# Kernel tuning notes

Measured on AMD Instinct MI355X. Metric: run time of the kernel, lower is better.

## Reference

```python
import jax, jax.numpy as jnp
import numpy as np

B, S, D, H = 4, 2048, 1024, 16
HD = D // H
SCALE = HD ** -0.5

def setup_inputs() -> dict:
    key = jax.random.key(0)
    k1, k2, k3 = jax.random.split(key, 3)
    x = jax.random.normal(k1, (B, S, D), dtype=jnp.float32)
    W_qkv = jax.random.normal(k2, (D, 3 * D), dtype=jnp.float32) * (D ** -0.5)
    b_qkv = jnp.zeros((3 * D,), dtype=jnp.float32)
    W_proj = jax.random.normal(k3, (D, D), dtype=jnp.float32) * (D ** -0.5)
    b_proj = jnp.zeros((D,), dtype=jnp.float32)
    return {"x": x, "W_qkv": W_qkv, "b_qkv": b_qkv, "W_proj": W_proj, "b_proj": b_proj}

def reference(x, W_qkv, b_qkv, W_proj, b_proj):
    # x: [B,S,D] -> qkv: [B,S,3D] -> [3,B,H,S,hd]
    qkv = x @ W_qkv + b_qkv
    qkv = qkv.reshape(B, S, 3, H, HD).transpose(2, 0, 3, 1, 4)
    q, k, v = qkv[0], qkv[1], qkv[2]
    # naive full attention: [B,H,S,S]
    attn = jnp.einsum('bhqd,bhkd->bhqk', q, k) * SCALE
    attn = jax.nn.softmax(attn, axis=-1)
    out = jnp.einsum('bhqk,bhkd->bhqd', attn, v)
    out = out.transpose(0, 2, 1, 3).reshape(B, S, D)
    return out @ W_proj + b_proj
```

## Files before the change

kernel.cpp:

```cpp
#include <hip/hip_runtime.h>

typedef __bf16 bf16x8 __attribute__((ext_vector_type(8)));
typedef unsigned short ushort8 __attribute__((ext_vector_type(8)));
typedef float floatx4 __attribute__((ext_vector_type(4)));
typedef unsigned int uintx4 __attribute__((ext_vector_type(4)));

__device__ __forceinline__ unsigned short f2bf(float f) {
  unsigned int u = __builtin_bit_cast(unsigned int, f);
  u += 0x7fffu + ((u >> 16) & 1u);
  return (unsigned short)(u >> 16);
}
__device__ __forceinline__ unsigned int pkbf(float a, float b) {
  unsigned int r;
  asm("v_cvt_pk_bf16_f32 %0, %1, %2" : "=v"(r) : "v"(a), "v"(b));
  return r;
}
__device__ __forceinline__ floatx4 MFMA16(bf16x8 a, bf16x8 b, floatx4 c) {
  return __builtin_amdgcn_mfma_f32_16x16x32_bf16(a, b, c, 0, 0, 0);
}

#define GLOAD16(gsrc, ldst)                                                  \
  __builtin_amdgcn_global_load_lds(                                          \
      (const __attribute__((address_space(1))) void*)(gsrc),                 \
      (__attribute__((address_space(3))) void*)(ldst), 16, 0, 0)

__global__ __launch_bounds__(256) void fill_f32(
    float* __restrict__ out, float val, size_t n) {
  const size_t t = (size_t)blockIdx.x * 256 + threadIdx.x;
  for (size_t i = t; i < n; i += (size_t)gridDim.x * 256) out[i] = val;
}

__global__ __launch_bounds__(256) void cvt_f32_bf16(
    const float* __restrict__ in, unsigned short* __restrict__ out) {
  const size_t t = (size_t)blockIdx.x * 256 + threadIdx.x;
  const float4 a = ((const float4*)in)[2 * t];
  const float4 b = ((const float4*)in)[2 * t + 1];
  uintx4 u;
  u[0] = pkbf(a.x, a.y); u[1] = pkbf(a.z, a.w);
  u[2] = pkbf(b.x, b.y); u[3] = pkbf(b.z, b.w);
  *(uintx4*)&out[t * 8] = u;
}

__global__ __launch_bounds__(256) void transpose_w(
    const float* __restrict__ in, unsigned short* __restrict__ out, int C) {
  __shared__ float T[64][65];
  const int tid = threadIdx.x;
  const int r0 = blockIdx.y * 64, c0 = blockIdx.x * 64;
#pragma unroll
  for (int e = 0; e < 4; ++e) {
    const int idx = e * 256 + tid;
    const int row = idx >> 4, cg = idx & 15;
    const float4 f = *(const float4*)&in[(size_t)(r0 + row) * C + c0 + cg * 4];
    T[row][cg * 4] = f.x; T[row][cg * 4 + 1] = f.y;
    T[row][cg * 4 + 2] = f.z; T[row][cg * 4 + 3] = f.w;
  }
  __syncthreads();
#pragma unroll
  for (int e = 0; e < 2; ++e) {
    const int idx = e * 256 + tid;
    const int cc = idx >> 3, rg = idx & 7;
    uintx4 u;
#pragma unroll
    for (int k = 0; k < 4; ++k)
      u[k] = pkbf(T[rg * 8 + 2 * k][cc], T[rg * 8 + 2 * k + 1][cc]);
    *(uintx4*)&out[(size_t)(c0 + cc) * 1024 + r0 + rg * 8] = u;
  }
}

template <int NBX, int EPI>
__global__ __launch_bounds__(512) void gemm8p(
    const unsigned short* __restrict__ A, const unsigned short* __restrict__ Bt,
    const float* __restrict__ bias, unsigned short* __restrict__ o0,
    unsigned short* __restrict__ o1, unsigned short* __restrict__ o2,
    float* __restrict__ of) {
  __shared__ __align__(16) unsigned short As[3][256 * 64];
  __shared__ __align__(16) unsigned short Bs[3][128 * 64];
  const int tid = threadIdx.x;
  const int lane = tid & 63;
  const int w = tid >> 6;
  const int g = lane >> 4, l15 = lane & 15;
  const int wr = w >> 1, wc = w & 1;
  constexpr int QX = 4 * NBX;
  const int orig = blockIdx.x;
  const int wgid = (orig & 7) * QX + (orig >> 3);
  const int m0 = (wgid / NBX) * 256, n0 = (wgid % NBX) * 128;

  floatx4 acc[4][4];
#pragma unroll
  for (int i = 0; i < 4; ++i)
#pragma unroll
    for (int j = 0; j < 4; ++j) acc[i][j] = {0.f, 0.f, 0.f, 0.f};

  const unsigned short* asrc[4];
  const unsigned short* bsrc[2];
  int adst[4], bdst[2];
#pragma unroll
  for (int p = 0; p < 4; ++p) {
    const int j = p * 512 + tid;
    const int row = j >> 3, G = j & 7;
    asrc[p] = A + (size_t)(m0 + row) * 1024 + (size_t)(G ^ (row & 7)) * 8;
    adst[p] = (j & ~63) * 8;
  }
#pragma unroll
  for (int p = 0; p < 2; ++p) {
    const int q = p * 512 + tid;
    const int row = q >> 3, G = q & 7;
    bsrc[p] = Bt + (size_t)(n0 + row) * 1024 + (size_t)(G ^ (row & 7)) * 8;
    bdst[p] = (q & ~63) * 8;
  }

  unsigned aoff[4][2], boff[4][2];
#pragma unroll
  for (int i = 0; i < 4; ++i) {
    const int ra = wr * 64 + i * 16 + l15;
    const int rb = wc * 64 + i * 16 + l15;
#pragma unroll
    for (int kh = 0; kh < 2; ++kh) {
      aoff[i][kh] = ra * 128 + (((kh * 4 + g) ^ (ra & 7)) * 16);
      boff[i][kh] = rb * 128 + (((kh * 4 + g) ^ (rb & 7)) * 16);
    }
  }

  auto STAGE = [&](int buf, int k0) {
#pragma unroll
    for (int p = 0; p < 4; ++p) GLOAD16(asrc[p] + k0, &As[buf][adst[p]]);
#pragma unroll
    for (int p = 0; p < 2; ++p) GLOAD16(bsrc[p] + k0, &Bs[buf][bdst[p]]);
  };
  auto COMPUTE = [&](int buf) {
    const char* ab = (const char*)As + buf * 32768;
    const char* bb = (const char*)Bs + buf * 16384;
#pragma unroll
    for (int kh = 0; kh < 2; ++kh) {
      bf16x8 af[4], bfr[4];
#pragma unroll
      for (int i = 0; i < 4; ++i) af[i] = *(const bf16x8*)(ab + aoff[i][kh]);
#pragma unroll
      for (int j = 0; j < 4; ++j) bfr[j] = *(const bf16x8*)(bb + boff[j][kh]);
      __builtin_amdgcn_s_setprio(1);
#pragma unroll
      for (int i = 0; i < 4; ++i)
#pragma unroll
        for (int j = 0; j < 4; ++j) acc[i][j] = MFMA16(af[i], bfr[j], acc[i][j]);
      __builtin_amdgcn_s_setprio(0);
    }
  };

  STAGE(0, 0);
  STAGE(1, 64);
#pragma unroll 1
  for (int t = 0; t < 16; ++t) {
    if (t < 14)
      asm volatile("s_waitcnt vmcnt(6)" ::: "memory");
    else
      asm volatile("s_waitcnt vmcnt(0)" ::: "memory");
    __builtin_amdgcn_s_barrier();
    if (t + 2 < 16) STAGE((t + 2) % 3, (t + 2) * 64);
    COMPUTE(t % 3);
    __builtin_amdgcn_s_barrier();
  }

#pragma unroll
  for (int i = 0; i < 4; ++i) {
#pragma unroll
    for (int j = 0; j < 4; ++j) {
      const int n = n0 + wc * 64 + j * 16 + l15;
      const float bv = bias[n];
      float vv[4];
#pragma unroll
      for (int r = 0; r < 4; ++r) vv[r] = acc[i][j][r] + bv;
      const int mb = m0 + wr * 64 + i * 16 + g * 4;
      if (EPI == 0) {
        const int three = n >> 10, h = (n >> 6) & 15, hd = n & 63;
        const int b = mb >> 11, s = mb & 2047;
        if (three == 2) {
          ushort4 pk;
          pk.x = f2bf(vv[0]); pk.y = f2bf(vv[1]);
          pk.z = f2bf(vv[2]); pk.w = f2bf(vv[3]);
          const int half = (s >> 5) & 1, hi16 = (s >> 4) & 1, gg = (s >> 2) & 3;
          const int col = (s & ~63) + (half * 4 + gg) * 8 + hi16 * 4;
          *(ushort4*)&o2[(((size_t)(b * 16 + h)) * 64 + hd) * 2048 + col] = pk;
        } else {
          const size_t idx0 = (((size_t)(b * 16 + h)) * 2048 + s) * 64 + hd;
#pragma unroll
          for (int r = 0; r < 4; ++r) {
            if (three == 0)
              o0[idx0 + (size_t)r * 64] = f2bf(vv[r] * 0.1803368801f);
            else
              o1[idx0 + (size_t)r * 64] = f2bf(vv[r]);
          }
        }
      } else {
#pragma unroll
        for (int r = 0; r < 4; ++r) of[(size_t)(mb + r) * 1024 + n] = vv[r];
      }
    }
  }
}

__global__ __launch_bounds__(512, 4) void attn_fwd(
    const unsigned short* __restrict__ Q, const unsigned short* __restrict__ Kq,
    const unsigned short* __restrict__ Vt, unsigned short* __restrict__ Ao) {
  __shared__ __align__(16) unsigned short Ks[2][4096];
  __shared__ __align__(16) unsigned short Vs[2][4096];
  const int blk = blockIdx.x;
  const int xcd = blk & 7, idx = blk >> 3;
  const int bh = xcd + 8 * (idx >> 3);
  const int qt = idx & 7;
  const int tid = threadIdx.x;
  const int lane = tid & 63;
  const int w = tid >> 6;
  const int g = lane >> 4, l15 = lane & 15;
  const int q0 = qt * 256 + w * 32;
  const unsigned short* Qp = Q + (size_t)bh * 2048 * 64;
  const unsigned short* Kp = Kq + (size_t)bh * 2048 * 64;
  const unsigned short* Vp = Vt + (size_t)bh * 64 * 2048;

  bf16x8 qf[2][2];
#pragma unroll
  for (int qg = 0; qg < 2; ++qg)
#pragma unroll
    for (int dh = 0; dh < 2; ++dh)
      qf[qg][dh] =
          *(const bf16x8*)&Qp[(size_t)(q0 + qg * 16 + l15) * 64 + dh * 32 + g * 8];

  const floatx4 minit = {-24.f, -24.f, -24.f, -24.f};
  const ushort8 onesu = {0x3F80, 0x3F80, 0x3F80, 0x3F80,
                         0x3F80, 0x3F80, 0x3F80, 0x3F80};
  const bf16x8 onesf = __builtin_bit_cast(bf16x8, onesu);
  floatx4 o[2][4], ol[2];
#pragma unroll
  for (int qg = 0; qg < 2; ++qg) {
#pragma unroll
    for (int tl = 0; tl < 4; ++tl) o[qg][tl] = {0.f, 0.f, 0.f, 0.f};
    ol[qg] = {0.f, 0.f, 0.f, 0.f};
  }

  const int x7 = l15 & 7;
  unsigned koffb[2];
#pragma unroll
  for (int dh = 0; dh < 2; ++dh)
    koffb[dh] = l15 * 128 + (((dh * 4 + g) ^ x7) * 16);
  const char* ksbase = (const char*)&Ks[0][0];
  const char* vsbase = (const char*)&Vs[0][0];

  const int j = tid;
  const int jsrc = (j & ~7) | ((j & 7) ^ ((j >> 3) & 7));
  const unsigned short* ksrc = Kp + jsrc * 8;
  const int vrow = j >> 3, sg = j & 7;
  const unsigned short* vsrc = Vp + (size_t)vrow * 2048 + (size_t)(sg ^ (vrow & 7)) * 8;
  const int dsto = (tid & ~63) * 8;

#define STAGE(BUF, kv0)                                                       \
  do {                                                                        \
    GLOAD16(ksrc + (size_t)(kv0) * 64, &Ks[BUF][dsto]);                       \
    GLOAD16(vsrc + (kv0), &Vs[BUF][dsto]);                                    \
  } while (0)

#define COMPUTE(BUF)                                                          \
  do {                                                                        \
    floatx4 s[2][4];                                                          \
    __builtin_amdgcn_s_setprio(1);                                            \
    _Pragma("unroll") for (int kvf = 0; kvf < 4; ++kvf) {                     \
      bf16x8 kf0 = *(const bf16x8*)(ksbase + (BUF)*8192 + kvf * 2048 +        \
                                    koffb[0]);                                \
      bf16x8 kf1 = *(const bf16x8*)(ksbase + (BUF)*8192 + kvf * 2048 +        \
                                    koffb[1]);                                \
      _Pragma("unroll") for (int qg = 0; qg < 2; ++qg) {                      \
        s[qg][kvf] = MFMA16(kf0, qf[qg][0], minit);                           \
        s[qg][kvf] = MFMA16(kf1, qf[qg][1], s[qg][kvf]);                      \
      }                                                                       \
    }                                                                         \
    __builtin_amdgcn_s_setprio(0);                                            \
    bf16x8 pf[2][2];                                                          \
    _Pragma("unroll") for (int qg = 0; qg < 2; ++qg) {                        \
      float p[4][4];                                                          \
      _Pragma("unroll") for (int kvf = 0; kvf < 4; ++kvf)                     \
          _Pragma("unroll") for (int r = 0; r < 4; ++r) p[kvf][r] =           \
          exp2f(s[qg][kvf][r]);                                               \
      uintx4 wa, wb;                                                          \
      wa[0] = pkbf(p[0][0], p[0][1]); wa[1] = pkbf(p[0][2], p[0][3]);         \
      wa[2] = pkbf(p[1][0], p[1][1]); wa[3] = pkbf(p[1][2], p[1][3]);         \
      wb[0] = pkbf(p[2][0], p[2][1]); wb[1] = pkbf(p[2][2], p[2][3]);         \
      wb[2] = pkbf(p[3][0], p[3][1]); wb[3] = pkbf(p[3][2], p[3][3]);         \
      pf[qg][0] = __builtin_bit_cast(bf16x8, wa);                             \
      pf[qg][1] = __builtin_bit_cast(bf16x8, wb);                             \
    }                                                                         \
    __builtin_amdgcn_s_setprio(1);                                            \
    ol[0] = MFMA16(pf[0][0], onesf, ol[0]);                                   \
    ol[0] = MFMA16(pf[0][1], onesf, ol[0]);                                   \
    ol[1] = MFMA16(pf[1][0], onesf, ol[1]);                                   \
    ol[1] = MFMA16(pf[1][1], onesf, ol[1]);                                   \
    _Pragma("unroll") for (int tl = 0; tl < 4; ++tl) {                        \
      _Pragma("unroll") for (int C = 0; C < 2; ++C) {                         \
        bf16x8 vf = *(const bf16x8*)(vsbase + (BUF)*8192 + tl * 2048 +        \
                                     koffb[C]);                               \
        o[0][tl] = MFMA16(pf[0][C], vf, o[0][tl]);                            \
        o[1][tl] = MFMA16(pf[1][C], vf, o[1][tl]);                            \
      }                                                                       \
    }                                                                         \
    __builtin_amdgcn_s_setprio(0);                                            \
  } while (0)

  STAGE(0, 0);
  __syncthreads();
#pragma unroll 1
  for (int t0 = 0; t0 < 32; t0 += 2) {
    STAGE(1, (t0 + 1) * 64);
    COMPUTE(0);
    __syncthreads();
    if (t0 + 2 < 32) STAGE(0, (t0 + 2) * 64);
    COMPUTE(1);
    __syncthreads();
  }
#undef STAGE
#undef COMPUTE

  const int b = bh >> 4, h = bh & 15;
#pragma unroll
  for (int qg = 0; qg < 2; ++qg) {
    float li[4];
#pragma unroll
    for (int r = 0; r < 4; ++r) li[r] = 1.0f / ol[qg][r];
#pragma unroll
    for (int tl = 0; tl < 4; ++tl)
#pragma unroll
      for (int r = 0; r < 4; ++r)
        Ao[((size_t)(b * 2048 + q0 + qg * 16 + g * 4 + r)) * 1024 + h * 64 +
           tl * 16 + l15] = f2bf(o[qg][tl][r] * li[r]);
  }
}

extern "C" void kernel_launch(void* const* d_in, const int* in_sizes, int n_in,
                              void* d_out, int out_size, void* d_ws, size_t ws_size,
                              hipStream_t stream) {
  float* outf = (float*)d_out;
  const size_t OUTN = (size_t)8192 * 1024;

  const float *x = nullptr, *Wqkv = nullptr, *bqkv = nullptr, *Wproj = nullptr,
              *bproj = nullptr;
  for (int i = 0; i < n_in; ++i) {
    switch (in_sizes[i]) {
      case 8388608: x = (const float*)d_in[i]; break;
      case 3145728: Wqkv = (const float*)d_in[i]; break;
      case 3072:    bqkv = (const float*)d_in[i]; break;
      case 1048576: Wproj = (const float*)d_in[i]; break;
      case 1024:    bproj = (const float*)d_in[i]; break;
      default: break;
    }
  }
  if (!x || !Wqkv || !bqkv || !Wproj || !bproj || n_in != 5) {
    fill_f32<<<2048, 256, 0, stream>>>(outf, 5000.0f, OUTN);
    return;
  }
  const size_t SZ = (size_t)4 * 16 * 2048 * 64 * 2;
  if (ws_size < 3 * SZ) {
    fill_f32<<<2048, 256, 0, stream>>>(outf, 1000.0f + (float)(ws_size >> 20), OUTN);
    return;
  }

  char* ws = (char*)d_ws;
  unsigned short* xb = (unsigned short*)(ws);
  unsigned short* Kb = (unsigned short*)(ws + SZ);
  unsigned short* Vtb = (unsigned short*)(ws + 2 * SZ);
  unsigned short* Qb = (unsigned short*)d_out;
  unsigned short* Wtq = (unsigned short*)((char*)d_out + SZ);
  unsigned short* Ao = xb;
  unsigned short* Wtp = Kb;

  cvt_f32_bf16<<<4096, 256, 0, stream>>>(x, xb);
  transpose_w<<<dim3(48, 16), 256, 0, stream>>>(Wqkv, Wtq, 3072);
  gemm8p<24, 0><<<768, 512, 0, stream>>>(
      xb, Wtq, bqkv, Qb, Kb, Vtb, nullptr);
  attn_fwd<<<512, 512, 0, stream>>>(Qb, Kb, Vtb, Ao);
  transpose_w<<<dim3(16, 16), 256, 0, stream>>>(Wproj, Wtp, 1024);
  gemm8p<8, 1><<<256, 512, 0, stream>>>(
      Ao, Wtp, bproj, nullptr, nullptr, nullptr, outf);
}
```

Baseline: 215.2 us.

## Split attention over KV halves with a merge kernel to double grid size

Splits each attention block's KV range into two halves, launching twice as many blocks that write fp32 partial outputs and row sums to workspace. A separate merge kernel sums the two partials, normalizes, and writes bf16 output. This aims to improve CU occupancy and load balance, at the cost of extra global memory traffic for the fp32 partials and an additional launch. It only runs when the workspace is large enough, otherwise it falls back to the original path.

```diff
diff --git a/kernel.cpp b/kernel.cpp
--- a/kernel.cpp
+++ b/kernel.cpp
@@ -198,15 +198,25 @@
   }
 }
 
+template <int SPLIT>
 __global__ __launch_bounds__(512, 4) void attn_fwd(
     const unsigned short* __restrict__ Q, const unsigned short* __restrict__ Kq,
-    const unsigned short* __restrict__ Vt, unsigned short* __restrict__ Ao) {
+    const unsigned short* __restrict__ Vt, unsigned short* __restrict__ Ao,
+    float* __restrict__ po, float* __restrict__ pol) {
   __shared__ __align__(16) unsigned short Ks[2][4096];
   __shared__ __align__(16) unsigned short Vs[2][4096];
   const int blk = blockIdx.x;
   const int xcd = blk & 7, idx = blk >> 3;
-  const int bh = xcd + 8 * (idx >> 3);
-  const int qt = idx & 7;
+  int bh, qt, kvh;
+  if (SPLIT) {
+    bh = xcd + 8 * (idx >> 4);
+    qt = (idx & 15) >> 1;
+    kvh = idx & 1;
+  } else {
+    bh = xcd + 8 * (idx >> 3);
+    qt = idx & 7;
+    kvh = 0;
+  }
   const int tid = threadIdx.x;
   const int lane = tid & 63;
   const int w = tid >> 6;
@@ -246,9 +256,10 @@
 
   const int j = tid;
   const int jsrc = (j & ~7) | ((j & 7) ^ ((j >> 3) & 7));
-  const unsigned short* ksrc = Kp + jsrc * 8;
+  const unsigned short* ksrc = Kp + (size_t)kvh * 1024 * 64 + jsrc * 8;
   const int vrow = j >> 3, sg = j & 7;
-  const unsigned short* vsrc = Vp + (size_t)vrow * 2048 + (size_t)(sg ^ (vrow & 7)) * 8;
+  const unsigned short* vsrc =
+      Vp + (size_t)vrow * 2048 + kvh * 1024 + (size_t)(sg ^ (vrow & 7)) * 8;
   const int dsto = (tid & ~63) * 8;
 
 #define STAGE(BUF, kv0)                                                       \
@@ -302,33 +313,72 @@
     __builtin_amdgcn_s_setprio(0);                                            \
   } while (0)
 
+  const int NT = SPLIT ? 16 : 32;
   STAGE(0, 0);
   __syncthreads();
 #pragma unroll 1
-  for (int t0 = 0; t0 < 32; t0 += 2) {
+  for (int t0 = 0; t0 < NT; t0 += 2) {
     STAGE(1, (t0 + 1) * 64);
     COMPUTE(0);
     __syncthreads();
-    if (t0 + 2 < 32) STAGE(0, (t0 + 2) * 64);
+    if (t0 + 2 < NT) STAGE(0, (t0 + 2) * 64);
     COMPUTE(1);
     __syncthreads();
   }
 #undef STAGE
 #undef COMPUTE
 
+  if (SPLIT) {
+    float* pob = po + (size_t)kvh * 8388608 + ((size_t)bh * 2048 + q0) * 64;
+    float* polb = pol + (size_t)kvh * 131072 + (size_t)bh * 2048 + q0;
+#pragma unroll
+    for (int qg = 0; qg < 2; ++qg) {
+#pragma unroll
+      for (int tl = 0; tl < 4; ++tl)
+#pragma unroll
+        for (int r = 0; r < 4; ++r)
+          pob[(size_t)(qg * 16 + g * 4 + r) * 64 + tl * 16 + l15] = o[qg][tl][r];
+      if (l15 == 0)
+#pragma unroll
+        for (int r = 0; r < 4; ++r) polb[qg * 16 + g * 4 + r] = ol[qg][r];
+    }
+  } else {
+    const int b = bh >> 4, h = bh & 15;
+#pragma unroll
+    for (int qg = 0; qg < 2; ++qg) {
+      float li[4];
+#pragma unroll
+      for (int r = 0; r < 4; ++r) li[r] = 1.0f / ol[qg][r];
+#pragma unroll
+      for (int tl = 0; tl < 4; ++tl)
+#pragma unroll
+        for (int r = 0; r < 4; ++r)
+          Ao[((size_t)(b * 2048 + q0 + qg * 16 + g * 4 + r)) * 1024 + h * 64 +
+             tl * 16 + l15] = f2bf(o[qg][tl][r] * li[r]);
+    }
+  }
+}
+
+__global__ __launch_bounds__(256) void attn_merge(
+    const float* __restrict__ po, const float* __restrict__ pol,
+    unsigned short* __restrict__ Ao) {
+  const size_t t = (size_t)blockIdx.x * 256 + threadIdx.x;
+  const size_t base = t * 8;
+  const size_t row = base >> 6;
+  const int d0 = (int)(base & 63);
+  const float4 a0 = *(const float4*)&po[base];
+  const float4 a1 = *(const float4*)&po[base + 4];
+  const float4 b0 = *(const float4*)&po[base + 8388608];
+  const float4 b1 = *(const float4*)&po[base + 8388608 + 4];
+  const float inv = 1.0f / (pol[row] + pol[row + 131072]);
+  uintx4 u;
+  u[0] = pkbf((a0.x + b0.x) * inv, (a0.y + b0.y) * inv);
+  u[1] = pkbf((a0.z + b0.z) * inv, (a0.w + b0.w) * inv);
+  u[2] = pkbf((a1.x + b1.x) * inv, (a1.y + b1.y) * inv);
+  u[3] = pkbf((a1.z + b1.z) * inv, (a1.w + b1.w) * inv);
+  const int bh = (int)(row >> 11), q = (int)(row & 2047);
   const int b = bh >> 4, h = bh & 15;
-#pragma unroll
-  for (int qg = 0; qg < 2; ++qg) {
-    float li[4];
-#pragma unroll
-    for (int r = 0; r < 4; ++r) li[r] = 1.0f / ol[qg][r];
-#pragma unroll
-    for (int tl = 0; tl < 4; ++tl)
-#pragma unroll
-      for (int r = 0; r < 4; ++r)
-        Ao[((size_t)(b * 2048 + q0 + qg * 16 + g * 4 + r)) * 1024 + h * 64 +
-           tl * 16 + l15] = f2bf(o[qg][tl][r] * li[r]);
-  }
+  *(uintx4*)&Ao[((size_t)(b * 2048 + q)) * 1024 + h * 64 + d0] = u;
 }
 
 extern "C" void kernel_launch(void* const* d_in, const int* in_sizes, int n_in,
@@ -368,11 +418,21 @@
   unsigned short* Ao = xb;
   unsigned short* Wtp = Kb;
 
+  float* po = (float*)(ws + 3 * SZ);
+  float* pol = (float*)(ws + 3 * SZ + 2 * 33554432ull);
+  const size_t NEED = 3 * SZ + 2 * 33554432ull + 2 * 524288ull;
+  const bool split = ws_size >= NEED;
+
   cvt_f32_bf16<<<4096, 256, 0, stream>>>(x, xb);
   transpose_w<<<dim3(48, 16), 256, 0, stream>>>(Wqkv, Wtq, 3072);
   gemm8p<24, 0><<<768, 512, 0, stream>>>(
       xb, Wtq, bqkv, Qb, Kb, Vtb, nullptr);
-  attn_fwd<<<512, 512, 0, stream>>>(Qb, Kb, Vtb, Ao);
+  if (split) {
+    attn_fwd<1><<<1024, 512, 0, stream>>>(Qb, Kb, Vtb, nullptr, po, pol);
+    attn_merge<<<4096, 256, 0, stream>>>(po, pol, Ao);
+  } else {
+    attn_fwd<0><<<512, 512, 0, stream>>>(Qb, Kb, Vtb, Ao, nullptr, nullptr);
+  }
   transpose_w<<<dim3(16, 16), 256, 0, stream>>>(Wproj, Wtp, 1024);
   gemm8p<8, 1><<<256, 512, 0, stream>>>(
       Ao, Wtp, bproj, nullptr, nullptr, nullptr, outf);
```

Result: slower. 225.2 us (+4.7%).
